# Optimization experiments

Measured on AMD Instinct MI355X. Metric: run time of the kernel, lower is better.

## Reference

```python
import jax, jax.numpy as jnp
import numpy as np

R = 8192            # reservoir_size
CORE = int(R * 0.6)          # 4915
SHELL = int(R * 0.3)         # 2457
FB = R - CORE - SHELL        # 820
H = 1024            # lstm_hidden
IN = 1              # input_size
OUT = 1             # output_size
LEAK = 0.1
SPECTRAL = 0.9
SPARSITY = 0.3


def _scaled(key, n):
    # uniform(-1,1) NxN; spectral radius of such a matrix ~ sqrt(n * var) = sqrt(n/3).
    # Scale to ~SPECTRAL (mimics the SVD-based scaling at init without the O(n^3) SVD).
    W = jax.random.uniform(key, (n, n), jnp.float32, -1.0, 1.0)
    return W * (SPECTRAL / jnp.sqrt(n / 3.0))


def setup_inputs() -> dict:
    key = jax.random.key(0)
    ks = jax.random.split(key, 20)
    u = lambda k, sh: jax.random.uniform(k, sh, jnp.float32, -1.0, 1.0)

    W_in = u(ks[0], (R, IN))
    W_core = _scaled(ks[1], CORE)
    mask_shell = (jax.random.uniform(ks[2], (SHELL, SHELL)) < SPARSITY).astype(jnp.float32)
    W_shell = _scaled(ks[3], SHELL) * mask_shell
    W_feedback = _scaled(ks[4], FB)
    W_shell_core = u(ks[5], (CORE, SHELL))
    W_feedback_core = u(ks[6], (CORE, FB))
    dopamine = jnp.float32(0.5)
    omega = jnp.ones((R,), jnp.float32) * 2.0
    gamma = jnp.ones((R,), jnp.float32) * 0.1

    # PyTorch LSTM params, gate order [i, f, g, o]
    s = 1.0 / np.sqrt(H)
    W_ih = jax.random.uniform(ks[7], (4 * H, R), jnp.float32, -s, s)
    W_hh = jax.random.uniform(ks[8], (4 * H, H), jnp.float32, -s, s)
    b_ih = jax.random.uniform(ks[9], (4 * H,), jnp.float32, -s, s)
    b_hh = jax.random.uniform(ks[10], (4 * H,), jnp.float32, -s, s)

    W_out = jax.random.uniform(ks[11], (OUT, H), jnp.float32, -s, s)
    b_out = jax.random.uniform(ks[12], (OUT,), jnp.float32, -s, s)

    x = jax.random.normal(ks[13], (IN,), jnp.float32)
    state = jax.random.normal(ks[14], (1, R), jnp.float32)
    lstm_hidden = jax.random.normal(ks[15], (1, 1, H), jnp.float32)
    lstm_cell = jax.random.normal(ks[16], (1, 1, H), jnp.float32)

    return dict(x=x, state=state, lstm_hidden=lstm_hidden, lstm_cell=lstm_cell,
                W_in=W_in, W_core=W_core, W_shell=W_shell, W_feedback=W_feedback,
                W_shell_core=W_shell_core, W_feedback_core=W_feedback_core,
                dopamine=dopamine, omega=omega, gamma=gamma,
                W_ih=W_ih, W_hh=W_hh, b_ih=b_ih, b_hh=b_hh,
                W_out=W_out, b_out=b_out)


def reference(x, state, lstm_hidden, lstm_cell,
              W_in, W_core, W_shell, W_feedback, W_shell_core, W_feedback_core,
              dopamine, omega, gamma, W_ih, W_hh, b_ih, b_hh, W_out, b_out):
    reservoir_in = W_in @ x                      # (R,)
    core = state[:, :CORE]                       # (1, CORE)
    shell = state[:, CORE:CORE + SHELL]          # (1, SHELL)
    fb = state[:, -FB:]                          # (1, FB)

    core_pred = jnp.tanh(core @ W_core.T + reservoir_in[:CORE][None, :])
    shell_pred = jnp.tanh(shell @ W_shell.T)
    fb_pred = jnp.tanh(fb @ W_feedback.T)
    core_pred = core_pred + jnp.tanh(shell_pred @ W_shell_core.T) \
                          + jnp.tanh(fb_pred @ W_feedback_core.T)

    core_new = (1.0 - LEAK) * core + LEAK * core_pred
    shell_new = (1.0 - LEAK) * shell + LEAK * shell_pred
    fb_new = (1.0 - LEAK) * fb + LEAK * fb_pred
    s = jnp.concatenate([core_new, shell_new, fb_new], axis=1)  # (1, R)

    # harmonic oscillator update + dopamine scaling
    s = s + 0.1 * (omega * s - gamma * jnp.tanh(s))
    s = dopamine * s

    # single LSTM cell step (torch gate order i, f, g, o)
    h = lstm_hidden[0]  # (1, H)
    c = lstm_cell[0]    # (1, H)
    gates = s @ W_ih.T + b_ih + h @ W_hh.T + b_hh   # (1, 4H)
    i, f, g, o = jnp.split(gates, 4, axis=1)
    c_new = jax.nn.sigmoid(f) * c + jax.nn.sigmoid(i) * jnp.tanh(g)
    h_new = jax.nn.sigmoid(o) * jnp.tanh(c_new)

    output = h_new @ W_out.T + b_out             # (1, OUT)
    return output, s, h_new[None], c_new[None]
```

## Files before the change

### kernel.cpp

```cpp
#include <hip/hip_runtime.h>
#include <hip/hip_bf16.h>
#include <math.h>

#define R_TOT 8192
#define CORE  4915
#define SHELL 2457
#define FB    820
#define H     1024

typedef unsigned short u16;
typedef __attribute__((ext_vector_type(8))) unsigned short ushort8v;

__device__ float g_pred1[R_TOT];
__device__ float g_s[R_TOT];
__device__ float g_gates[4 * H];
__device__ unsigned int g_isF32;

__device__ __forceinline__ float bf2f(u16 u) {
  union { unsigned int i; float f; } v; v.i = ((unsigned int)u) << 16; return v.f;
}

template <bool F32>
__device__ __forceinline__ float ld(const void* p, int i) {
  if (F32) return ((const float*)p)[i];
  else     return bf2f(((const u16*)p)[i]);
}

template <bool F32>
__device__ __forceinline__ void st(void* p, int i, float v) {
  if (F32) ((float*)p)[i] = v;
  else     ((__hip_bfloat16*)p)[i] = __float2bfloat16(v);
}

__device__ __forceinline__ float waveReduce(float v) {
  #pragma unroll
  for (int off = 32; off; off >>= 1) v += __shfl_down(v, off, 64);
  return v;
}

template <bool F32>
__device__ __forceinline__ float dotRow(const void* w_, const float* __restrict__ xs,
                                        int N, int lane) {
  float sum = 0.f;
  if (F32) {
    const float* w = (const float*)w_;
    uintptr_t a = (uintptr_t)w;
    int head = (int)(((16 - (a & 15)) & 15) >> 2);
    if (head > N) head = N;
    if (lane < head) sum += w[lane] * xs[lane];
    int nC = (N - head) >> 2;
    const float4* wv = (const float4*)(w + head);
    for (int c = lane; c < nC; c += 64) {
      float4 v = wv[c];
      int base = head + (c << 2);
      sum += v.x * xs[base] + v.y * xs[base + 1] + v.z * xs[base + 2] + v.w * xs[base + 3];
    }
    for (int i = head + (nC << 2) + lane; i < N; i += 64) sum += w[i] * xs[i];
  } else {
    const u16* w = (const u16*)w_;
    uintptr_t a = (uintptr_t)w;
    int head = (int)(((16 - (a & 15)) & 15) >> 1);
    if (head > N) head = N;
    if (lane < head) sum += bf2f(w[lane]) * xs[lane];
    int nC = (N - head) >> 3;
    const ushort8v* wv = (const ushort8v*)(w + head);
    for (int c = lane; c < nC; c += 64) {
      ushort8v v = wv[c];
      int base = head + (c << 3);
      #pragma unroll
      for (int k = 0; k < 8; ++k) sum += bf2f(v[k]) * xs[base + k];
    }
    for (int i = head + (nC << 3) + lane; i < N; i += 64) sum += bf2f(w[i]) * xs[i];
  }
  return sum;
}

__global__ void k_detect(const unsigned int* __restrict__ omega_words) {
  if (threadIdx.x == 0) g_isF32 = (omega_words[0] == 0x40000000u) ? 1u : 0u;
}

#define NB1_CORE  ((CORE  + 3) / 4)
#define NB1_SHELL ((SHELL + 3) / 4)
#define NB1_FB    ((FB    + 3) / 4)

template <bool F32>
__device__ __forceinline__ void stage1_body(
    const void* state, const void* Wcore, const void* Wshell, const void* Wfb,
    const void* Win, const void* xin, float* xs) {
  int b = blockIdx.x;
  int rowBase, N, xoff, isCore = 0;
  const void* W;
  const size_t esz = F32 ? 4 : 2;
  if (b < NB1_CORE)                { rowBase = b * 4;                        N = CORE;  xoff = 0;            W = Wcore; isCore = 1; }
  else if (b < NB1_CORE+NB1_SHELL) { rowBase = (b - NB1_CORE) * 4;           N = SHELL; xoff = CORE;         W = Wshell; }
  else                             { rowBase = (b - NB1_CORE - NB1_SHELL)*4; N = FB;    xoff = CORE + SHELL; W = Wfb; }
  for (int i = threadIdx.x; i < N; i += 256) xs[i] = ld<F32>(state, xoff + i);
  __syncthreads();
  int wave = threadIdx.x >> 6, lane = threadIdx.x & 63;
  int r = rowBase + wave;
  if (r >= N) return;
  const void* row = (const void*)((const char*)W + (size_t)r * N * esz);
  float sum = waveReduce(dotRow<F32>(row, xs, N, lane));
  if (lane == 0) {
    if (isCore) sum += ld<F32>(Win, r) * ld<F32>(xin, 0);
    g_pred1[xoff + r] = tanhf(sum);
  }
}

__global__ __launch_bounds__(256) void k_stage1(
    const void* state, const void* Wcore, const void* Wshell, const void* Wfb,
    const void* Win, const void* xin) {
  __shared__ float xs[CORE];
  if (g_isF32) stage1_body<true>(state, Wcore, Wshell, Wfb, Win, xin, xs);
  else         stage1_body<false>(state, Wcore, Wshell, Wfb, Win, xin, xs);
}

#define NB2_CORE ((CORE + 3) / 4)
#define NB2_EW   ((SHELL + FB + 255) / 256)

template <bool F32>
__device__ __forceinline__ void s_update(int i, float pred, const void* state,
                                         const void* omega, const void* gamma,
                                         float dopa, void* dout) {
  float old = ld<F32>(state, i);
  float s1 = 0.9f * old + 0.1f * pred;
  float s2 = s1 + 0.1f * (ld<F32>(omega, i) * s1 - ld<F32>(gamma, i) * tanhf(s1));
  float s3 = dopa * s2;
  g_s[i] = s3;
  st<F32>(dout, 1 + i, s3);
}

template <bool F32>
__device__ __forceinline__ void stage2_body(
    const void* state, const void* Wsc, const void* Wfc,
    const void* omega, const void* gamma, const void* dopamine,
    void* dout, float* xs) {
  float dopa = ld<F32>(dopamine, 0);
  int b = blockIdx.x;
  const size_t esz = F32 ? 4 : 2;
  if (b < NB2_CORE) {
    for (int i = threadIdx.x; i < SHELL + FB; i += 256) xs[i] = g_pred1[CORE + i];
    __syncthreads();
    int wave = threadIdx.x >> 6, lane = threadIdx.x & 63;
    int r = b * 4 + wave;
    if (r >= CORE) return;
    const void* row1 = (const void*)((const char*)Wsc + (size_t)r * SHELL * esz);
    const void* row2 = (const void*)((const char*)Wfc + (size_t)r * FB * esz);
    float d1 = waveReduce(dotRow<F32>(row1, xs, SHELL, lane));
    float d2 = waveReduce(dotRow<F32>(row2, xs + SHELL, FB, lane));
    if (lane == 0) {
      float pred = g_pred1[r] + tanhf(d1) + tanhf(d2);
      s_update<F32>(r, pred, state, omega, gamma, dopa, dout);
    }
  } else {
    int i = CORE + (b - NB2_CORE) * 256 + threadIdx.x;
    if (i < R_TOT) s_update<F32>(i, g_pred1[i], state, omega, gamma, dopa, dout);
  }
}

__global__ __launch_bounds__(256) void k_stage2(
    const void* state, const void* Wsc, const void* Wfc,
    const void* omega, const void* gamma, const void* dopamine, void* dout) {
  __shared__ float xs[SHELL + FB];
  if (g_isF32) stage2_body<true>(state, Wsc, Wfc, omega, gamma, dopamine, dout, xs);
  else         stage2_body<false>(state, Wsc, Wfc, omega, gamma, dopamine, dout, xs);
}

template <bool F32>
__device__ __forceinline__ void gates_body(
    const void* h, const void* Wih, const void* Whh,
    const void* bih, const void* bhh, float* xs) {
  const size_t esz = F32 ? 4 : 2;
  for (int i = threadIdx.x; i < R_TOT; i += 256) xs[i] = g_s[i];
  for (int i = threadIdx.x; i < H; i += 256) xs[R_TOT + i] = ld<F32>(h, i);
  __syncthreads();
  int wave = threadIdx.x >> 6, lane = threadIdx.x & 63;
  int r = blockIdx.x * 4 + wave;
  const void* row1 = (const void*)((const char*)Wih + (size_t)r * R_TOT * esz);
  const void* row2 = (const void*)((const char*)Whh + (size_t)r * H * esz);
  float sum = dotRow<F32>(row1, xs, R_TOT, lane)
            + dotRow<F32>(row2, xs + R_TOT, H, lane);
  sum = waveReduce(sum);
  if (lane == 0) g_gates[r] = sum + ld<F32>(bih, r) + ld<F32>(bhh, r);
}

__global__ __launch_bounds__(256) void k_gates(
    const void* h, const void* Wih, const void* Whh,
    const void* bih, const void* bhh) {
  __shared__ float xs[R_TOT + H];
  if (g_isF32) gates_body<true>(h, Wih, Whh, bih, bhh, xs);
  else         gates_body<false>(h, Wih, Whh, bih, bhh, xs);
}

template <bool F32>
__device__ __forceinline__ void lstm_body(
    const void* c_in, const void* Wout, const void* bout, void* dout, float* red) {
  int j = threadIdx.x;
  float ig = g_gates[j], fg = g_gates[H + j], gg = g_gates[2 * H + j], og = g_gates[3 * H + j];
  float c = ld<F32>(c_in, j);
  float cn = (1.f / (1.f + expf(-fg))) * c + (1.f / (1.f + expf(-ig))) * tanhf(gg);
  float hn = (1.f / (1.f + expf(-og))) * tanhf(cn);
  st<F32>(dout, 1 + R_TOT + j, hn);
  st<F32>(dout, 1 + R_TOT + H + j, cn);
  float w = ld<F32>(Wout, j) * hn;
  w = waveReduce(w);
  int wave = j >> 6, lane = j & 63;
  if (lane == 0) red[wave] = w;
  __syncthreads();
  if (j == 0) {
    float t = 0.f;
    #pragma unroll
    for (int k = 0; k < 16; ++k) t += red[k];
    st<F32>(dout, 0, t + ld<F32>(bout, 0));
  }
}

__global__ __launch_bounds__(1024) void k_lstm(
    const void* c_in, const void* Wout, const void* bout, void* dout) {
  __shared__ float red[16];
  if (g_isF32) lstm_body<true>(c_in, Wout, bout, dout, red);
  else         lstm_body<false>(c_in, Wout, bout, dout, red);
}

extern "C" void kernel_launch(void* const* d_in, const int* in_sizes, int n_in,
                              void* d_out, int out_size, void* d_ws, size_t ws_size,
                              hipStream_t stream) {
  const void *x = 0, *state = 0, *h = 0, *c = 0, *Win = 0, *Wcore = 0, *Wshell = 0,
             *Wfb = 0, *Wsc = 0, *Wfc = 0, *dopa = 0, *omega = 0, *gamma = 0,
             *Wih = 0, *Whh = 0, *bih = 0, *bhh = 0, *Wout = 0, *bout = 0;
  int n1 = 0, n1024 = 0, n8192 = 0, n4096 = 0;
  for (int i = 0; i < n_in; ++i) {
    const void* p = d_in[i];
    switch (in_sizes[i]) {
      case 24157225: Wcore = p; break;
      case 6036849:  Wshell = p; break;
      case 672400:   Wfb = p; break;
      case 12076155: Wsc = p; break;
      case 4030300:  Wfc = p; break;
      case 33554432: Wih = p; break;
      case 4194304:  Whh = p; break;
      case 1:    { if (n1 == 0) x = p; else if (n1 == 1) dopa = p; else bout = p; n1++; } break;
      case 1024: { if (n1024 == 0) h = p; else if (n1024 == 1) c = p; else Wout = p; n1024++; } break;
      case 8192: { if (n8192 == 0) state = p; else if (n8192 == 1) Win = p;
                   else if (n8192 == 2) omega = p; else gamma = p; n8192++; } break;
      case 4096: { if (n4096 == 0) bih = p; else bhh = p; n4096++; } break;
      default: break;
    }
  }

  k_detect<<<1, 64, 0, stream>>>((const unsigned int*)omega);
  k_stage1<<<NB1_CORE + NB1_SHELL + NB1_FB, 256, 0, stream>>>(
      state, Wcore, Wshell, Wfb, Win, x);
  k_stage2<<<NB2_CORE + NB2_EW, 256, 0, stream>>>(
      state, Wsc, Wfc, omega, gamma, dopa, d_out);
  k_gates<<<(4 * H) / 4, 256, 0, stream>>>(h, Wih, Whh, bih, bhh);
  k_lstm<<<1, 1024, 0, stream>>>(c, Wout, bout, d_out);
}
```

Baseline: 371.6 us.

## Drop bf16 path, unroll float4 row loads, pad shared vector against bank conflicts

Removes the runtime dtype-detection kernel and the bf16 template branches, hard-coding fp32 inputs. The dot-product loop is unrolled to issue four independent float4 loads per lane with separate accumulators, giving more memory-level parallelism on the bandwidth-bound GEMV. The shared-memory x vector is padded by one element every 32 to avoid LDS bank conflicts from lanes reading stride-4 elements. Launch bounds gain occupancy hints. It drops one launch but no longer handles bf16 inputs.

New measurement: 369.1 us. Within noise of the previous version (-0.7%).

```diff
diff --git a/kernel.cpp b/kernel.cpp
--- a/kernel.cpp
+++ b/kernel.cpp
@@ -1,5 +1,4 @@
 #include <hip/hip_runtime.h>
-#include <hip/hip_bf16.h>
 #include <math.h>
 
 #define R_TOT 8192
@@ -8,29 +7,12 @@
 #define FB    820
 #define H     1024
 
-typedef unsigned short u16;
-typedef __attribute__((ext_vector_type(8))) unsigned short ushort8v;
-
 __device__ float g_pred1[R_TOT];
 __device__ float g_s[R_TOT];
 __device__ float g_gates[4 * H];
-__device__ unsigned int g_isF32;
 
-__device__ __forceinline__ float bf2f(u16 u) {
-  union { unsigned int i; float f; } v; v.i = ((unsigned int)u) << 16; return v.f;
-}
-
-template <bool F32>
-__device__ __forceinline__ float ld(const void* p, int i) {
-  if (F32) return ((const float*)p)[i];
-  else     return bf2f(((const u16*)p)[i]);
-}
-
-template <bool F32>
-__device__ __forceinline__ void st(void* p, int i, float v) {
-  if (F32) ((float*)p)[i] = v;
-  else     ((__hip_bfloat16*)p)[i] = __float2bfloat16(v);
-}
+__device__ __forceinline__ int swz(int i) { return i + (i >> 5); }
+#define SWZ_SIZE(n) ((n) + (((n) - 1) >> 5))
 
 __device__ __forceinline__ float waveReduce(float v) {
   #pragma unroll
@@ -38,171 +20,133 @@
   return v;
 }
 
-template <bool F32>
-__device__ __forceinline__ float dotRow(const void* w_, const float* __restrict__ xs,
-                                        int N, int lane) {
-  float sum = 0.f;
-  if (F32) {
-    const float* w = (const float*)w_;
-    uintptr_t a = (uintptr_t)w;
-    int head = (int)(((16 - (a & 15)) & 15) >> 2);
-    if (head > N) head = N;
-    if (lane < head) sum += w[lane] * xs[lane];
-    int nC = (N - head) >> 2;
-    const float4* wv = (const float4*)(w + head);
-    for (int c = lane; c < nC; c += 64) {
-      float4 v = wv[c];
-      int base = head + (c << 2);
-      sum += v.x * xs[base] + v.y * xs[base + 1] + v.z * xs[base + 2] + v.w * xs[base + 3];
-    }
-    for (int i = head + (nC << 2) + lane; i < N; i += 64) sum += w[i] * xs[i];
-  } else {
-    const u16* w = (const u16*)w_;
-    uintptr_t a = (uintptr_t)w;
-    int head = (int)(((16 - (a & 15)) & 15) >> 1);
-    if (head > N) head = N;
-    if (lane < head) sum += bf2f(w[lane]) * xs[lane];
-    int nC = (N - head) >> 3;
-    const ushort8v* wv = (const ushort8v*)(w + head);
-    for (int c = lane; c < nC; c += 64) {
-      ushort8v v = wv[c];
-      int base = head + (c << 3);
-      #pragma unroll
-      for (int k = 0; k < 8; ++k) sum += bf2f(v[k]) * xs[base + k];
-    }
-    for (int i = head + (nC << 3) + lane; i < N; i += 64) sum += bf2f(w[i]) * xs[i];
+__device__ __forceinline__ float dotRow(const float* __restrict__ w,
+                                        const float* __restrict__ xs,
+                                        int xb, int N, int lane) {
+  uintptr_t a = (uintptr_t)w;
+  int head = (int)(((16 - (a & 15)) & 15) >> 2);
+  if (head > N) head = N;
+  float s0 = 0.f, s1 = 0.f, s2 = 0.f, s3 = 0.f;
+  if (lane < head) s0 += w[lane] * xs[swz(xb + lane)];
+  int nC = (N - head) >> 2;
+  const float4* wv = (const float4*)(w + head);
+  int b0 = xb + head;
+  int c = lane;
+  for (; c + 192 < nC; c += 256) {
+    float4 v0 = wv[c], v1 = wv[c + 64], v2 = wv[c + 128], v3 = wv[c + 192];
+    int i0 = b0 + (c << 2);
+    s0 += v0.x*xs[swz(i0    )] + v0.y*xs[swz(i0+  1)] + v0.z*xs[swz(i0+  2)] + v0.w*xs[swz(i0+  3)];
+    s1 += v1.x*xs[swz(i0+256)] + v1.y*xs[swz(i0+257)] + v1.z*xs[swz(i0+258)] + v1.w*xs[swz(i0+259)];
+    s2 += v2.x*xs[swz(i0+512)] + v2.y*xs[swz(i0+513)] + v2.z*xs[swz(i0+514)] + v2.w*xs[swz(i0+515)];
+    s3 += v3.x*xs[swz(i0+768)] + v3.y*xs[swz(i0+769)] + v3.z*xs[swz(i0+770)] + v3.w*xs[swz(i0+771)];
   }
-  return sum;
-}
-
-__global__ void k_detect(const unsigned int* __restrict__ omega_words) {
-  if (threadIdx.x == 0) g_isF32 = (omega_words[0] == 0x40000000u) ? 1u : 0u;
+  for (; c < nC; c += 64) {
+    float4 v = wv[c];
+    int i0 = b0 + (c << 2);
+    s1 += v.x*xs[swz(i0)] + v.y*xs[swz(i0+1)] + v.z*xs[swz(i0+2)] + v.w*xs[swz(i0+3)];
+  }
+  for (int i = head + (nC << 2) + lane; i < N; i += 64)
+    s2 += w[i] * xs[swz(xb + i)];
+  return (s0 + s1) + (s2 + s3);
 }
 
 #define NB1_CORE  ((CORE  + 3) / 4)
 #define NB1_SHELL ((SHELL + 3) / 4)
 #define NB1_FB    ((FB    + 3) / 4)
 
-template <bool F32>
-__device__ __forceinline__ void stage1_body(
-    const void* state, const void* Wcore, const void* Wshell, const void* Wfb,
-    const void* Win, const void* xin, float* xs) {
+__global__ __launch_bounds__(256, 8) void k_stage1(
+    const float* __restrict__ state, const float* __restrict__ Wcore,
+    const float* __restrict__ Wshell, const float* __restrict__ Wfb,
+    const float* __restrict__ Win, const float* __restrict__ xin) {
+  __shared__ float xs[SWZ_SIZE(CORE)];
   int b = blockIdx.x;
   int rowBase, N, xoff, isCore = 0;
-  const void* W;
-  const size_t esz = F32 ? 4 : 2;
-  if (b < NB1_CORE)                { rowBase = b * 4;                        N = CORE;  xoff = 0;            W = Wcore; isCore = 1; }
-  else if (b < NB1_CORE+NB1_SHELL) { rowBase = (b - NB1_CORE) * 4;           N = SHELL; xoff = CORE;         W = Wshell; }
-  else                             { rowBase = (b - NB1_CORE - NB1_SHELL)*4; N = FB;    xoff = CORE + SHELL; W = Wfb; }
-  for (int i = threadIdx.x; i < N; i += 256) xs[i] = ld<F32>(state, xoff + i);
+  const float* W;
+  if (b < NB1_CORE)                  { rowBase = b * 4;                         N = CORE;  xoff = 0;            W = Wcore; isCore = 1; }
+  else if (b < NB1_CORE + NB1_SHELL) { rowBase = (b - NB1_CORE) * 4;            N = SHELL; xoff = CORE;         W = Wshell; }
+  else                               { rowBase = (b - NB1_CORE - NB1_SHELL)*4;  N = FB;    xoff = CORE + SHELL; W = Wfb; }
+  for (int i = threadIdx.x; i < N; i += 256) xs[swz(i)] = state[xoff + i];
   __syncthreads();
   int wave = threadIdx.x >> 6, lane = threadIdx.x & 63;
   int r = rowBase + wave;
   if (r >= N) return;
-  const void* row = (const void*)((const char*)W + (size_t)r * N * esz);
-  float sum = waveReduce(dotRow<F32>(row, xs, N, lane));
+  float sum = waveReduce(dotRow(W + (size_t)r * N, xs, 0, N, lane));
   if (lane == 0) {
-    if (isCore) sum += ld<F32>(Win, r) * ld<F32>(xin, 0);
+    if (isCore) sum += Win[r] * xin[0];
     g_pred1[xoff + r] = tanhf(sum);
   }
-}
-
-__global__ __launch_bounds__(256) void k_stage1(
-    const void* state, const void* Wcore, const void* Wshell, const void* Wfb,
-    const void* Win, const void* xin) {
-  __shared__ float xs[CORE];
-  if (g_isF32) stage1_body<true>(state, Wcore, Wshell, Wfb, Win, xin, xs);
-  else         stage1_body<false>(state, Wcore, Wshell, Wfb, Win, xin, xs);
 }
 
 #define NB2_CORE ((CORE + 3) / 4)
 #define NB2_EW   ((SHELL + FB + 255) / 256)
 
-template <bool F32>
-__device__ __forceinline__ void s_update(int i, float pred, const void* state,
-                                         const void* omega, const void* gamma,
-                                         float dopa, void* dout) {
-  float old = ld<F32>(state, i);
+__device__ __forceinline__ void s_update(int i, float pred,
+                                         const float* __restrict__ state,
+                                         const float* __restrict__ omega,
+                                         const float* __restrict__ gamma,
+                                         float dopa, float* __restrict__ dout) {
+  float old = state[i];
   float s1 = 0.9f * old + 0.1f * pred;
-  float s2 = s1 + 0.1f * (ld<F32>(omega, i) * s1 - ld<F32>(gamma, i) * tanhf(s1));
+  float s2 = s1 + 0.1f * (omega[i] * s1 - gamma[i] * tanhf(s1));
   float s3 = dopa * s2;
   g_s[i] = s3;
-  st<F32>(dout, 1 + i, s3);
+  dout[1 + i] = s3;
 }
 
-template <bool F32>
-__device__ __forceinline__ void stage2_body(
-    const void* state, const void* Wsc, const void* Wfc,
-    const void* omega, const void* gamma, const void* dopamine,
-    void* dout, float* xs) {
-  float dopa = ld<F32>(dopamine, 0);
+__global__ __launch_bounds__(256, 8) void k_stage2(
+    const float* __restrict__ state,
+    const float* __restrict__ Wsc, const float* __restrict__ Wfc,
+    const float* __restrict__ omega, const float* __restrict__ gamma,
+    const float* __restrict__ dopamine, float* __restrict__ dout) {
+  __shared__ float xs[SWZ_SIZE(SHELL + FB)];
+  float dopa = dopamine[0];
   int b = blockIdx.x;
-  const size_t esz = F32 ? 4 : 2;
   if (b < NB2_CORE) {
-    for (int i = threadIdx.x; i < SHELL + FB; i += 256) xs[i] = g_pred1[CORE + i];
+    for (int i = threadIdx.x; i < SHELL + FB; i += 256) xs[swz(i)] = g_pred1[CORE + i];
     __syncthreads();
     int wave = threadIdx.x >> 6, lane = threadIdx.x & 63;
     int r = b * 4 + wave;
     if (r >= CORE) return;
-    const void* row1 = (const void*)((const char*)Wsc + (size_t)r * SHELL * esz);
-    const void* row2 = (const void*)((const char*)Wfc + (size_t)r * FB * esz);
-    float d1 = waveReduce(dotRow<F32>(row1, xs, SHELL, lane));
-    float d2 = waveReduce(dotRow<F32>(row2, xs + SHELL, FB, lane));
+    float d1 = waveReduce(dotRow(Wsc + (size_t)r * SHELL, xs, 0, SHELL, lane));
+    float d2 = waveReduce(dotRow(Wfc + (size_t)r * FB, xs, SHELL, FB, lane));
     if (lane == 0) {
       float pred = g_pred1[r] + tanhf(d1) + tanhf(d2);
-      s_update<F32>(r, pred, state, omega, gamma, dopa, dout);
+      s_update(r, pred, state, omega, gamma, dopa, dout);
     }
   } else {
     int i = CORE + (b - NB2_CORE) * 256 + threadIdx.x;
-    if (i < R_TOT) s_update<F32>(i, g_pred1[i], state, omega, gamma, dopa, dout);
+    if (i < R_TOT) s_update(i, g_pred1[i], state, omega, gamma, dopa, dout);
   }
 }
 
-__global__ __launch_bounds__(256) void k_stage2(
-    const void* state, const void* Wsc, const void* Wfc,
-    const void* omega, const void* gamma, const void* dopamine, void* dout) {
-  __shared__ float xs[SHELL + FB];
-  if (g_isF32) stage2_body<true>(state, Wsc, Wfc, omega, gamma, dopamine, dout, xs);
-  else         stage2_body<false>(state, Wsc, Wfc, omega, gamma, dopamine, dout, xs);
-}
-
-template <bool F32>
-__device__ __forceinline__ void gates_body(
-    const void* h, const void* Wih, const void* Whh,
-    const void* bih, const void* bhh, float* xs) {
-  const size_t esz = F32 ? 4 : 2;
-  for (int i = threadIdx.x; i < R_TOT; i += 256) xs[i] = g_s[i];
-  for (int i = threadIdx.x; i < H; i += 256) xs[R_TOT + i] = ld<F32>(h, i);
+__global__ __launch_bounds__(256, 4) void k_gates(
+    const float* __restrict__ h,
+    const float* __restrict__ Wih, const float* __restrict__ Whh,
+    const float* __restrict__ bih, const float* __restrict__ bhh) {
+  __shared__ float xs[SWZ_SIZE(R_TOT + H)];
+  for (int i = threadIdx.x; i < R_TOT; i += 256) xs[swz(i)] = g_s[i];
+  for (int i = threadIdx.x; i < H; i += 256) xs[swz(R_TOT + i)] = h[i];
   __syncthreads();
   int wave = threadIdx.x >> 6, lane = threadIdx.x & 63;
   int r = blockIdx.x * 4 + wave;
-  const void* row1 = (const void*)((const char*)Wih + (size_t)r * R_TOT * esz);
-  const void* row2 = (const void*)((const char*)Whh + (size_t)r * H * esz);
-  float sum = dotRow<F32>(row1, xs, R_TOT, lane)
-            + dotRow<F32>(row2, xs + R_TOT, H, lane);
+  float sum = dotRow(Wih + (size_t)r * R_TOT, xs, 0, R_TOT, lane)
+            + dotRow(Whh + (size_t)r * H, xs, R_TOT, H, lane);
   sum = waveReduce(sum);
-  if (lane == 0) g_gates[r] = sum + ld<F32>(bih, r) + ld<F32>(bhh, r);
+  if (lane == 0) g_gates[r] = sum + bih[r] + bhh[r];
 }
 
-__global__ __launch_bounds__(256) void k_gates(
-    const void* h, const void* Wih, const void* Whh,
-    const void* bih, const void* bhh) {
-  __shared__ float xs[R_TOT + H];
-  if (g_isF32) gates_body<true>(h, Wih, Whh, bih, bhh, xs);
-  else         gates_body<false>(h, Wih, Whh, bih, bhh, xs);
-}
-
-template <bool F32>
-__device__ __forceinline__ void lstm_body(
-    const void* c_in, const void* Wout, const void* bout, void* dout, float* red) {
+__global__ __launch_bounds__(1024) void k_lstm(
+    const float* __restrict__ c_in, const float* __restrict__ Wout,
+    const float* __restrict__ bout, float* __restrict__ dout) {
+  __shared__ float red[16];
   int j = threadIdx.x;
   float ig = g_gates[j], fg = g_gates[H + j], gg = g_gates[2 * H + j], og = g_gates[3 * H + j];
-  float c = ld<F32>(c_in, j);
+  float c = c_in[j];
   float cn = (1.f / (1.f + expf(-fg))) * c + (1.f / (1.f + expf(-ig))) * tanhf(gg);
   float hn = (1.f / (1.f + expf(-og))) * tanhf(cn);
-  st<F32>(dout, 1 + R_TOT + j, hn);
-  st<F32>(dout, 1 + R_TOT + H + j, cn);
-  float w = ld<F32>(Wout, j) * hn;
+  dout[1 + R_TOT + j] = hn;
+  dout[1 + R_TOT + H + j] = cn;
+  float w = Wout[j] * hn;
   w = waveReduce(w);
   int wave = j >> 6, lane = j & 63;
   if (lane == 0) red[wave] = w;
@@ -211,26 +155,19 @@
     float t = 0.f;
     #pragma unroll
     for (int k = 0; k < 16; ++k) t += red[k];
-    st<F32>(dout, 0, t + ld<F32>(bout, 0));
+    dout[0] = t + bout[0];
   }
-}
-
-__global__ __launch_bounds__(1024) void k_lstm(
-    const void* c_in, const void* Wout, const void* bout, void* dout) {
-  __shared__ float red[16];
-  if (g_isF32) lstm_body<true>(c_in, Wout, bout, dout, red);
-  else         lstm_body<false>(c_in, Wout, bout, dout, red);
 }
 
 extern "C" void kernel_launch(void* const* d_in, const int* in_sizes, int n_in,
                               void* d_out, int out_size, void* d_ws, size_t ws_size,
                               hipStream_t stream) {
-  const void *x = 0, *state = 0, *h = 0, *c = 0, *Win = 0, *Wcore = 0, *Wshell = 0,
-             *Wfb = 0, *Wsc = 0, *Wfc = 0, *dopa = 0, *omega = 0, *gamma = 0,
-             *Wih = 0, *Whh = 0, *bih = 0, *bhh = 0, *Wout = 0, *bout = 0;
+  const float *x = 0, *state = 0, *h = 0, *c = 0, *Win = 0, *Wcore = 0, *Wshell = 0,
+              *Wfb = 0, *Wsc = 0, *Wfc = 0, *dopa = 0, *omega = 0, *gamma = 0,
+              *Wih = 0, *Whh = 0, *bih = 0, *bhh = 0, *Wout = 0, *bout = 0;
   int n1 = 0, n1024 = 0, n8192 = 0, n4096 = 0;
   for (int i = 0; i < n_in; ++i) {
-    const void* p = d_in[i];
+    const float* p = (const float*)d_in[i];
     switch (in_sizes[i]) {
       case 24157225: Wcore = p; break;
       case 6036849:  Wshell = p; break;
@@ -247,12 +184,12 @@
       default: break;
     }
   }
+  float* dout = (float*)d_out;
 
-  k_detect<<<1, 64, 0, stream>>>((const unsigned int*)omega);
   k_stage1<<<NB1_CORE + NB1_SHELL + NB1_FB, 256, 0, stream>>>(
       state, Wcore, Wshell, Wfb, Win, x);
   k_stage2<<<NB2_CORE + NB2_EW, 256, 0, stream>>>(
-      state, Wsc, Wfc, omega, gamma, dopa, d_out);
+      state, Wsc, Wfc, omega, gamma, dopa, dout);
   k_gates<<<(4 * H) / 4, 256, 0, stream>>>(h, Wih, Whh, bih, bhh);
-  k_lstm<<<1, 1024, 0, stream>>>(c, Wout, bout, d_out);
+  k_lstm<<<1, 1024, 0, stream>>>(c, Wout, bout, dout);
 }
```
